# Kernel optimization log

Hardware: AMD Instinct MI355X
Metric: run time of the kernel (lower is better)

## Reference

```python
import jax, jax.numpy as jnp
import numpy as np

B, C, N, L, LAYERS = 32, 128, 307, 12, 4
LH = L + 1  # high-frequency channel time length after left-pad
BN_EPS = 1e-5


def _temporal_attention(seq, c1w, c2w, w, b, v, gamma, beta):
    # seq: [B, C, N, T]
    # conv1 (1x1 over channel dim) -> f1: [B, T, N]
    f1 = jnp.einsum('bcnt,c->btn', seq, c1w)
    # conv2 (1x1 over node dim)    -> f2: [B, T, C]
    f2 = jnp.einsum('bcnt,n->btc', seq, c2w)
    # scores = sigmoid(f1 @ w @ f2^T + b): [B, T, T]
    f1w = jnp.einsum('btn,nc->btc', f1, w)
    scores = jax.nn.sigmoid(jnp.einsum('btc,bqc->btq', f1w, f2) + b)
    # learned mixing: v @ scores
    logits = jnp.einsum('tk,bkq->btq', v, scores)
    # BatchNorm1d over tem_size channels (channel = last axis q after the
    # permute(0,2,1) in the torch code); training-mode batch statistics
    mean = logits.mean(axis=(0, 1), keepdims=True)
    var = ((logits - mean) ** 2).mean(axis=(0, 1), keepdims=True)
    logits = (logits - mean) * jax.lax.rsqrt(var + BN_EPS) * gamma + beta
    coefs = jax.nn.softmax(logits, axis=-1)  # [B, T, Q]
    # x_1 = einsum('bcnl,blq->bcnq', seq, coefs^T)
    return jnp.einsum('bcnt,bqt->bcnq', seq, coefs)


def _make_params(key, c, n, t, layers):
    ks = jax.random.split(key, 4)
    return dict(
        c1=jax.random.normal(ks[0], (layers, c), jnp.float32) * 0.05,
        c2=jax.random.normal(ks[1], (layers, n), jnp.float32) * 0.05,
        w=jax.random.normal(ks[2], (layers, n, c), jnp.float32) * 0.05,
        b=jnp.zeros((layers, t, t), jnp.float32),
        v=jax.random.normal(ks[3], (layers, t, t), jnp.float32) * 0.2,
        g=jnp.ones((layers, t), jnp.float32),
        beta=jnp.zeros((layers, t), jnp.float32),
    )


def setup_inputs():
    key = jax.random.key(0)
    k0, k1, k2, k3 = jax.random.split(key, 4)
    XL = jax.random.normal(k0, (B, C, N, L), jnp.float32)
    XH = jax.random.normal(k1, (B, C, N, L), jnp.float32)
    low = _make_params(k2, C, N, L, LAYERS)
    high = _make_params(k3, C, N, LH, LAYERS)
    return {
        'XL': XL, 'XH': XH,
        'low_c1': low['c1'], 'low_c2': low['c2'], 'low_w': low['w'],
        'low_b': low['b'], 'low_v': low['v'], 'low_g': low['g'], 'low_beta': low['beta'],
        'high_c1': high['c1'], 'high_c2': high['c2'], 'high_w': high['w'],
        'high_b': high['b'], 'high_v': high['v'], 'high_g': high['g'], 'high_beta': high['beta'],
        'alpha': jnp.array(-5.0, jnp.float32),
    }


def reference(XL, XH, low_c1, low_c2, low_w, low_b, low_v, low_g, low_beta,
              high_c1, high_c2, high_w, high_b, high_v, high_g, high_beta, alpha):
    res_xl, res_xh = XL, XH
    x = XL
    for i in range(LAYERS):
        x = _temporal_attention(x, low_c1[i], low_c2[i], low_w[i], low_b[i],
                                low_v[i], low_g[i], low_beta[i])
    xl = (res_xl[..., -1] + x[..., -1])[..., None]  # [B, C, N, 1]

    y = jnp.pad(XH, ((0, 0), (0, 0), (0, 0), (1, 0)))  # left-pad time -> [B,C,N,L+1]
    for i in range(LAYERS):
        y = _temporal_attention(y, high_c1[i], high_c2[i], high_w[i], high_b[i],
                                high_v[i], high_g[i], high_beta[i])
    xh = (res_xh[..., -1] + y[..., -1])[..., None]  # [B, C, N, 1]

    a = jax.nn.sigmoid(alpha)
    return a * xl + (1.0 - a) * xh
```

## Files before the change

kernel.cpp:

```cpp
#include <hip/hip_runtime.h>

#define Bn 32
#define Cc 128
#define Nn 307
#define Ll 12
#define LH 13
#define LAYERS 4
#define BN_EPS 1e-5f
#define SCW (Cc + 1)
#define G1SZ ((size_t)2 * LAYERS * Bn * LH * Nn)

#define NT1 16
__global__ __launch_bounds__(256, 4) void k_g1(const float* __restrict__ XL,
                                               const float* __restrict__ XH,
                                               const float* __restrict__ lc1,
                                               const float* __restrict__ hc1,
                                               float* __restrict__ G1) {
    __shared__ float s_c1[LAYERS * Cc];
    __shared__ float sred[12 * 260];
    int tile = blockIdx.x;
    int b = blockIdx.y;
    int ch = blockIdx.z;
    const float* X = ch ? XH : XL;
    const float* c1 = ch ? hc1 : lc1;
    int tid = threadIdx.x;
    for (int j = tid; j < LAYERS * Cc; j += 256) s_c1[j] = c1[j];
    __syncthreads();
    int nl = tid & 15;
    int l = (tid >> 4) & 3;
    int cs = tid >> 6;
    int n = tile * NT1 + nl;
    float4 a0 = {0.f, 0.f, 0.f, 0.f}, a1 = a0, a2 = a0;
    if (n < Nn) {
        const float* px = X + ((size_t)(b * Cc + cs * 32) * Nn + n) * Ll;
        const float* wp = s_c1 + l * Cc + cs * 32;
#pragma unroll 4
        for (int cc = 0; cc < 32; ++cc) {
            float4 v0 = *(const float4*)(px);
            float4 v1 = *(const float4*)(px + 4);
            float4 v2 = *(const float4*)(px + 8);
            float wv = wp[cc];
            a0.x += v0.x * wv; a0.y += v0.y * wv; a0.z += v0.z * wv; a0.w += v0.w * wv;
            a1.x += v1.x * wv; a1.y += v1.y * wv; a1.z += v1.z * wv; a1.w += v1.w * wv;
            a2.x += v2.x * wv; a2.y += v2.y * wv; a2.z += v2.z * wv; a2.w += v2.w * wv;
            px += (size_t)Nn * Ll;
        }
    }
    int g = tid & 63;
    float av[12] = {a0.x, a0.y, a0.z, a0.w, a1.x, a1.y,
                    a1.z, a1.w, a2.x, a2.y, a2.z, a2.w};
#pragma unroll
    for (int t = 0; t < 12; ++t) sred[t * 260 + cs * 64 + g] = av[t];
    __syncthreads();
#pragma unroll
    for (int r = 0; r < 3; ++r) {
        int o = r * 256 + tid;
        int og = o & 63, t = o >> 6;
        float v = sred[t * 260 + og] + sred[t * 260 + 64 + og] +
                  sred[t * 260 + 128 + og] + sred[t * 260 + 192 + og];
        int onl = og & 15, ol = og >> 4;
        int nn = tile * NT1 + onl;
        int t0 = ch ? (t + 1) : t;
        if (nn < Nn)
            G1[((size_t)(ch * LAYERS + ol) * Bn + b) * (LH * Nn) + (size_t)t0 * Nn + nn] = v;
    }
    if (tid < 64) {
        int onl = tid & 15, ol = tid >> 4;
        int nn = tile * NT1 + onl;
        int t0z = ch ? 0 : (LH - 1);
        if (nn < Nn)
            G1[((size_t)(ch * LAYERS + ol) * Bn + b) * (LH * Nn) + (size_t)t0z * Nn + nn] = 0.f;
    }
}

__global__ __launch_bounds__(256, 4) void k_g2(const float* __restrict__ XL,
                                               const float* __restrict__ XH,
                                               const float* __restrict__ lc2,
                                               const float* __restrict__ hc2,
                                               float* __restrict__ G2) {
    __shared__ float s_c2[LAYERS * Nn];
    __shared__ float sred[12 * 260];
    int ctile = blockIdx.x;
    int b = blockIdx.y;
    int ch = blockIdx.z;
    const float* X = ch ? XH : XL;
    const float* c2 = ch ? hc2 : lc2;
    int tid = threadIdx.x;
    for (int j = tid; j < LAYERS * Nn; j += 256) s_c2[j] = c2[j];
    __syncthreads();
    int c8 = tid & 7;
    int l = (tid >> 3) & 3;
    int ns = tid >> 5;
    int c = ctile * 8 + c8;
    float4 a0 = {0.f, 0.f, 0.f, 0.f}, a1 = a0, a2 = a0;
    const float* pb = X + (size_t)(b * Cc + c) * Nn * Ll;
    const float* wp = s_c2 + l * Nn;
#pragma unroll 4
    for (int n = ns; n < Nn; n += 8) {
        const float* px = pb + (size_t)n * Ll;
        float4 v0 = *(const float4*)(px);
        float4 v1 = *(const float4*)(px + 4);
        float4 v2 = *(const float4*)(px + 8);
        float wv = wp[n];
        a0.x += v0.x * wv; a0.y += v0.y * wv; a0.z += v0.z * wv; a0.w += v0.w * wv;
        a1.x += v1.x * wv; a1.y += v1.y * wv; a1.z += v1.z * wv; a1.w += v1.w * wv;
        a2.x += v2.x * wv; a2.y += v2.y * wv; a2.z += v2.z * wv; a2.w += v2.w * wv;
    }
    float av[12] = {a0.x, a0.y, a0.z, a0.w, a1.x, a1.y,
                    a1.z, a1.w, a2.x, a2.y, a2.z, a2.w};
#pragma unroll
    for (int t = 0; t < 12; ++t) sred[t * 260 + tid] = av[t];
    __syncthreads();
    size_t cb;
#pragma unroll
    for (int r = 0; r < 2; ++r) {
        int o = r * 256 + tid;
        if (o < 384) {
            int og = o & 31, t = o >> 5;
            float v = 0.f;
#pragma unroll
            for (int s = 0; s < 8; ++s) v += sred[t * 260 + s * 32 + og];
            int oc8 = og & 7, ol = og >> 3;
            int t0 = ch ? (t + 1) : t;
            G2[((size_t)(ch * LAYERS + ol) * Bn + b) * (LH * Cc) + (size_t)t0 * Cc +
               ctile * 8 + oc8] = v;
        }
    }
    if (ch && tid < 32) {
        int oc8 = tid & 7, ol = tid >> 3;
        G2[((size_t)(ch * LAYERS + ol) * Bn + b) * (LH * Cc) + ctile * 8 + oc8] = 0.f;
    }
}

#define GWR 4
__global__ __launch_bounds__(256) void k_gw(const float* __restrict__ lw,
                                            const float* __restrict__ hw,
                                            const float* __restrict__ G1,
                                            float* __restrict__ GW) {
    __shared__ float sG1[GWR * Nn];
    __shared__ float sred[8][GWR][Cc];
    int tile = blockIdx.x;
    int chl = blockIdx.y;
    int ch = chl >> 2, l = chl & 3;
    const float* w = (ch ? hw : lw) + (size_t)l * Nn * Cc;
    const float* g1 = G1 + (size_t)chl * Bn * (LH * Nn) + (size_t)tile * GWR * Nn;
    int tid = threadIdx.x;
    for (int i = tid; i < GWR * Nn / 4; i += 256)
        ((float4*)sG1)[i] = ((const float4*)g1)[i];
    __syncthreads();
    int c4 = (tid & 31) * 4;
    int stripe = tid >> 5;
    float4 a0 = {0.f, 0.f, 0.f, 0.f}, a1 = a0, a2 = a0, a3 = a0;
#define GW_FMA(wv, nn)                                         \
    {                                                          \
        float g0 = sG1[0 * Nn + (nn)];                         \
        float g1v = sG1[1 * Nn + (nn)];                        \
        float g2v = sG1[2 * Nn + (nn)];                        \
        float g3v = sG1[3 * Nn + (nn)];                        \
        a0.x += wv.x * g0;  a0.y += wv.y * g0;                 \
        a0.z += wv.z * g0;  a0.w += wv.w * g0;                 \
        a1.x += wv.x * g1v; a1.y += wv.y * g1v;                \
        a1.z += wv.z * g1v; a1.w += wv.w * g1v;                \
        a2.x += wv.x * g2v; a2.y += wv.y * g2v;                \
        a2.z += wv.z * g2v; a2.w += wv.w * g2v;                \
        a3.x += wv.x * g3v; a3.y += wv.y * g3v;                \
        a3.z += wv.z * g3v; a3.w += wv.w * g3v;                \
    }
    int n = stripe;
    for (; n + 24 < Nn; n += 32) {
        float4 w0 = *(const float4*)(w + (size_t)n * Cc + c4);
        float4 w1 = *(const float4*)(w + (size_t)(n + 8) * Cc + c4);
        float4 w2 = *(const float4*)(w + (size_t)(n + 16) * Cc + c4);
        float4 w3 = *(const float4*)(w + (size_t)(n + 24) * Cc + c4);
        GW_FMA(w0, n);
        GW_FMA(w1, n + 8);
        GW_FMA(w2, n + 16);
        GW_FMA(w3, n + 24);
    }
    for (; n < Nn; n += 8) {
        float4 w0 = *(const float4*)(w + (size_t)n * Cc + c4);
        GW_FMA(w0, n);
    }
#undef GW_FMA
    *(float4*)&sred[stripe][0][c4] = a0;
    *(float4*)&sred[stripe][1][c4] = a1;
    *(float4*)&sred[stripe][2][c4] = a2;
    *(float4*)&sred[stripe][3][c4] = a3;
    __syncthreads();
    float* out = GW + (size_t)chl * Bn * (LH * Cc) + (size_t)tile * GWR * Cc;
    for (int o = tid; o < GWR * Cc; o += 256) {
        int r = o >> 7, cc = o & 127;
        float v = 0.f;
#pragma unroll
        for (int s = 0; s < 8; ++s) v += sred[s][r][cc];
        out[o] = v;
    }
}

__global__ __launch_bounds__(256) void k_m(const float* __restrict__ GW,
                                           const float* __restrict__ G2,
                                           float* __restrict__ M) {
    __shared__ float sGW[LH][SCW];
    __shared__ float sG2[LH][SCW];
    int blk = blockIdx.x;
    int ch = blk >> 7;
    int T = ch ? LH : Ll;
    const float* gw = GW + (size_t)blk * (LH * Cc);
    const float* g2 = G2 + (size_t)blk * (LH * Cc);
    int tid = threadIdx.x;
    for (int i = tid; i < LH * Cc; i += 256) {
        int t = i >> 7, c = i & 127;
        sGW[t][c] = gw[i];
        sG2[t][c] = g2[i];
    }
    __syncthreads();
    float* Mo = M + (size_t)blk * (LH * LH);
    for (int i = tid; i < T * T; i += 256) {
        int t0 = i / T, t1 = i % T;
        float a = 0.f;
#pragma unroll 8
        for (int cc = 0; cc < Cc; ++cc) a += sGW[t0][cc] * sG2[t1][cc];
        Mo[t0 * LH + t1] = a;
    }
}

template <int T>
__device__ __forceinline__ void first_impl(int ch, int b,
                                           const float* __restrict__ M,
                                           const float* __restrict__ bb,
                                           const float* __restrict__ v,
                                           float* __restrict__ Lg,
                                           float* __restrict__ Stats) {
    const int TT = T * T;
    __shared__ float sS[LH * LH];
    __shared__ float sA[LH * LH];
    int tid = threadIdx.x;
    const float* Ml = M + ((size_t)(ch * LAYERS + 0) * Bn + b) * (LH * LH);
    if (tid < TT) {
        int t = tid / T, q = tid % T;
        float a = bb[tid] + Ml[t * LH + q];
        sS[tid] = 1.f / (1.f + expf(-a));
    }
    __syncthreads();
    if (tid < TT) {
        int t = tid / T, q = tid % T;
        float a = 0.f;
#pragma unroll
        for (int k = 0; k < T; ++k) a += v[t * T + k] * sS[k * T + q];
        sA[tid] = a;
        Lg[(size_t)(ch * Bn + b) * (LH * LH) + tid] = a;
    }
    __syncthreads();
    if (tid < T) {
        float s = 0.f, ss = 0.f;
#pragma unroll
        for (int t = 0; t < T; ++t) {
            float x = sA[t * T + tid];
            s += x;
            ss += x * x;
        }
        float* St = Stats + (size_t)(0 * 2 + ch) * 2 * (LH * Bn);
        St[tid * Bn + b] = s;
        St[LH * Bn + tid * Bn + b] = ss;
    }
}

__global__ __launch_bounds__(192) void k_first(const float* __restrict__ M,
                                               const float* __restrict__ lb,
                                               const float* __restrict__ lv,
                                               const float* __restrict__ hb,
                                               const float* __restrict__ hv,
                                               float* __restrict__ Lg,
                                               float* __restrict__ Stats) {
    int ch = blockIdx.x >> 5, b = blockIdx.x & 31;
    if (ch == 0)
        first_impl<Ll>(0, b, M, lb, lv, Lg, Stats);
    else
        first_impl<LH>(1, b, M, hb, hv, Lg, Stats);
}

template <int T>
__device__ __forceinline__ void mid_impl(int ch, int b, int l,
                                         const float* __restrict__ M,
                                         const float* __restrict__ bb_all,
                                         const float* __restrict__ v_all,
                                         const float* __restrict__ g_all,
                                         const float* __restrict__ be_all,
                                         float* __restrict__ Lg,
                                         float* __restrict__ Stats,
                                         float* __restrict__ Pws) {
    const int TT = T * T;
    __shared__ float sP[LH * LH], sC[LH * LH], sA[LH * LH], sB[LH * LH], sM[LH * LH];
    __shared__ float sMean[LH], sScale[LH], sShift[LH];
    int tid = threadIdx.x;
    bool first = (l == 0);
    float* Lgb = Lg + (size_t)(ch * Bn + b) * (LH * LH);
    float* Pb = Pws + (size_t)(ch * Bn + b) * (LH * LH);
    if (tid < T) {
        const float* St = Stats + (size_t)(l * 2 + ch) * 2 * (LH * Bn);
        float s = 0.f, ss = 0.f;
        for (int b2 = 0; b2 < Bn; ++b2) {
            s += St[tid * Bn + b2];
            ss += St[LH * Bn + tid * Bn + b2];
        }
        float inv = 1.f / (float)(Bn * T);
        float m = s * inv;
        float var = ss * inv - m * m;
        sMean[tid] = m;
        sScale[tid] = rsqrtf(var + BN_EPS) * g_all[l * T + tid];
        sShift[tid] = be_all[l * T + tid];
    }
    if (tid < TT) {
        sA[tid] = Lgb[tid];
        if (!first) sP[tid] = Pb[tid];
    }
    __syncthreads();
    if (tid < T) {
        float vals[T];
        float mx = -1e30f;
#pragma unroll
        for (int q = 0; q < T; ++q) {
            float x = (sA[tid * T + q] - sMean[q]) * sScale[q] + sShift[q];
            vals[q] = x;
            mx = fmaxf(mx, x);
        }
        float sm = 0.f;
#pragma unroll
        for (int q = 0; q < T; ++q) {
            vals[q] = expf(vals[q] - mx);
            sm += vals[q];
        }
        float inv = 1.f / sm;
#pragma unroll
        for (int q = 0; q < T; ++q) sC[tid * T + q] = vals[q] * inv;
    }
    __syncthreads();
    if (tid < TT) {
        int t0 = tid / T, q = tid % T;
        float a;
        if (first) {
            a = sC[q * T + t0];
        } else {
            a = 0.f;
#pragma unroll
            for (int t = 0; t < T; ++t) a += sP[t0 * T + t] * sC[q * T + t];
        }
        sB[tid] = a;
        Pb[tid] = a;
    }
    const float* Mn = M + ((size_t)(ch * LAYERS + l + 1) * Bn + b) * (LH * LH);
    for (int i = tid; i < T * LH; i += 192) sM[i] = Mn[i];
    __syncthreads();
    if (tid < TT) {
        int t = tid / T, t1 = tid % T;
        float a = 0.f;
#pragma unroll
        for (int t0 = 0; t0 < T; ++t0) a += sB[t0 * T + t] * sM[t0 * LH + t1];
        sA[tid] = a;
    }
    __syncthreads();
    const float* bbn = bb_all + (size_t)(l + 1) * TT;
    if (tid < TT) {
        int t = tid / T, q = tid % T;
        float a = bbn[tid];
#pragma unroll
        for (int t1 = 0; t1 < T; ++t1) a += sA[t * T + t1] * sB[t1 * T + q];
        sP[tid] = 1.f / (1.f + expf(-a));
    }
    __syncthreads();
    const float* vn = v_all + (size_t)(l + 1) * TT;
    if (tid < TT) {
        int t = tid / T, q = tid % T;
        float a = 0.f;
#pragma unroll
        for (int k = 0; k < T; ++k) a += vn[t * T + k] * sP[k * T + q];
        sA[tid] = a;
        Lgb[tid] = a;
    }
    __syncthreads();
    if (tid < T) {
        float s = 0.f, ss = 0.f;
#pragma unroll
        for (int t = 0; t < T; ++t) {
            float x = sA[t * T + tid];
            s += x;
            ss += x * x;
        }
        float* St = Stats + (size_t)((l + 1) * 2 + ch) * 2 * (LH * Bn);
        St[tid * Bn + b] = s;
        St[LH * Bn + tid * Bn + b] = ss;
    }
}

__global__ __launch_bounds__(192) void k_mid(const float* __restrict__ M,
                                             const float* __restrict__ lb,
                                             const float* __restrict__ lv,
                                             const float* __restrict__ lgam,
                                             const float* __restrict__ lbet,
                                             const float* __restrict__ hb,
                                             const float* __restrict__ hv,
                                             const float* __restrict__ hgam,
                                             const float* __restrict__ hbet,
                                             float* __restrict__ Lg,
                                             float* __restrict__ Stats,
                                             float* __restrict__ Pws, int l) {
    int ch = blockIdx.x >> 5, b = blockIdx.x & 31;
    if (ch == 0)
        mid_impl<Ll>(0, b, l, M, lb, lv, lgam, lbet, Lg, Stats, Pws);
    else
        mid_impl<LH>(1, b, l, M, hb, hv, hgam, hbet, Lg, Stats, Pws);
}

template <int T>
__device__ __forceinline__ void last_impl(int ch, int b,
                                          const float* __restrict__ g_all,
                                          const float* __restrict__ be_all,
                                          const float* __restrict__ Lg,
                                          const float* __restrict__ Stats,
                                          const float* __restrict__ Pws,
                                          float* __restrict__ Pcol) {
    const int TT = T * T;
    const int l = LAYERS - 1;
    __shared__ float sP[LH * LH], sC[LH * LH], sA[LH * LH], sB[LH * LH];
    __shared__ float sMean[LH], sScale[LH], sShift[LH];
    int tid = threadIdx.x;
    const float* Lgb = Lg + (size_t)(ch * Bn + b) * (LH * LH);
    const float* Pb = Pws + (size_t)(ch * Bn + b) * (LH * LH);
    if (tid < T) {
        const float* St = Stats + (size_t)(l * 2 + ch) * 2 * (LH * Bn);
        float s = 0.f, ss = 0.f;
        for (int b2 = 0; b2 < Bn; ++b2) {
            s += St[tid * Bn + b2];
            ss += St[LH * Bn + tid * Bn + b2];
        }
        float inv = 1.f / (float)(Bn * T);
        float m = s * inv;
        float var = ss * inv - m * m;
        sMean[tid] = m;
        sScale[tid] = rsqrtf(var + BN_EPS) * g_all[l * T + tid];
        sShift[tid] = be_all[l * T + tid];
    }
    if (tid < TT) {
        sA[tid] = Lgb[tid];
        sP[tid] = Pb[tid];
    }
    __syncthreads();
    if (tid < T) {
        float vals[T];
        float mx = -1e30f;
#pragma unroll
        for (int q = 0; q < T; ++q) {
            float x = (sA[tid * T + q] - sMean[q]) * sScale[q] + sShift[q];
            vals[q] = x;
            mx = fmaxf(mx, x);
        }
        float sm = 0.f;
#pragma unroll
        for (int q = 0; q < T; ++q) {
            vals[q] = expf(vals[q] - mx);
            sm += vals[q];
        }
        float inv = 1.f / sm;
#pragma unroll
        for (int q = 0; q < T; ++q) sC[tid * T + q] = vals[q] * inv;
    }
    __syncthreads();
    if (tid < TT) {
        int t0 = tid / T, q = tid % T;
        float a = 0.f;
#pragma unroll
        for (int t = 0; t < T; ++t) a += sP[t0 * T + t] * sC[q * T + t];
        sB[tid] = a;
    }
    __syncthreads();
    if (tid < T) Pcol[(size_t)ch * Bn * LH + b * LH + tid] = sB[tid * T + (T - 1)];
}

__global__ __launch_bounds__(192) void k_last(const float* __restrict__ lgam,
                                              const float* __restrict__ lbet,
                                              const float* __restrict__ hgam,
                                              const float* __restrict__ hbet,
                                              const float* __restrict__ Lg,
                                              const float* __restrict__ Stats,
                                              const float* __restrict__ Pws,
                                              float* __restrict__ Pcol) {
    int ch = blockIdx.x >> 5, b = blockIdx.x & 31;
    if (ch == 0)
        last_impl<Ll>(0, b, lgam, lbet, Lg, Stats, Pws, Pcol);
    else
        last_impl<LH>(1, b, hgam, hbet, Lg, Stats, Pws, Pcol);
}

__global__ __launch_bounds__(256) void k_final(const float* __restrict__ XL,
                                               const float* __restrict__ XH,
                                               const float* __restrict__ Pcol,
                                               const float* __restrict__ alpha,
                                               float* __restrict__ out) {
    __shared__ float s_pl[Ll];
    __shared__ float s_ph[LH];
    int b = blockIdx.y;
    int tid = threadIdx.x;
    if (tid < Ll) s_pl[tid] = Pcol[b * LH + tid];
    if (tid < LH) s_ph[tid] = Pcol[Bn * LH + b * LH + tid];
    __syncthreads();
    int cn = blockIdx.x * blockDim.x + tid;
    if (cn >= Cc * Nn) return;
    size_t idx = (size_t)b * Cc * Nn + cn;
    const float* pl = XL + idx * Ll;
    const float* ph = XH + idx * Ll;
    float accL = 0.f, accH = 0.f;
#pragma unroll
    for (int t = 0; t < Ll; ++t) {
        accL += pl[t] * s_pl[t];
        accH += ph[t] * s_ph[t + 1];
    }
    float a = 1.f / (1.f + expf(-alpha[0]));
    float xl = pl[Ll - 1] + accL;
    float xh = ph[Ll - 1] + accH;
    out[idx] = a * xl + (1.f - a) * xh;
}

extern "C" void kernel_launch(void* const* d_in, const int* in_sizes, int n_in,
                              void* d_out, int out_size, void* d_ws, size_t ws_size,
                              hipStream_t stream) {
    const float* XL = (const float*)d_in[0];
    const float* XH = (const float*)d_in[1];
    const float* lc1 = (const float*)d_in[2];
    const float* lc2 = (const float*)d_in[3];
    const float* lw = (const float*)d_in[4];
    const float* lb = (const float*)d_in[5];
    const float* lv = (const float*)d_in[6];
    const float* lg = (const float*)d_in[7];
    const float* lbeta = (const float*)d_in[8];
    const float* hc1 = (const float*)d_in[9];
    const float* hc2 = (const float*)d_in[10];
    const float* hw = (const float*)d_in[11];
    const float* hb = (const float*)d_in[12];
    const float* hv = (const float*)d_in[13];
    const float* hg = (const float*)d_in[14];
    const float* hbeta = (const float*)d_in[15];
    const float* alpha = (const float*)d_in[16];
    float* out = (float*)d_out;

    float* ws = (float*)d_ws;
    float* G1 = ws;
    float* G2 = G1 + G1SZ;
    float* M = G2 + (size_t)2 * LAYERS * Bn * LH * Cc;
    float* Pcol = M + (size_t)2 * LAYERS * Bn * LH * LH;
    float* Stats = Pcol + (size_t)2 * Bn * LH;
    float* Lg = Stats + (size_t)4 * LAYERS * LH * Bn;
    float* Pws = Lg + (size_t)2 * Bn * LH * LH;
    float* GW = Pws + (size_t)2 * Bn * LH * LH;

    k_g1<<<dim3(20, 32, 2), 256, 0, stream>>>(XL, XH, lc1, hc1, G1);
    k_g2<<<dim3(16, 32, 2), 256, 0, stream>>>(XL, XH, lc2, hc2, G2);
    k_gw<<<dim3(104, 8), 256, 0, stream>>>(lw, hw, G1, GW);
    k_m<<<256, 256, 0, stream>>>(GW, G2, M);
    k_first<<<64, 192, 0, stream>>>(M, lb, lv, hb, hv, Lg, Stats);
    k_mid<<<64, 192, 0, stream>>>(M, lb, lv, lg, lbeta, hb, hv, hg, hbeta, Lg, Stats, Pws, 0);
    k_mid<<<64, 192, 0, stream>>>(M, lb, lv, lg, lbeta, hb, hv, hg, hbeta, Lg, Stats, Pws, 1);
    k_mid<<<64, 192, 0, stream>>>(M, lb, lv, lg, lbeta, hb, hv, hg, hbeta, Lg, Stats, Pws, 2);
    k_last<<<64, 192, 0, stream>>>(lg, lbeta, hg, hbeta, Lg, Stats, Pws, Pcol);
    k_final<<<dim3((Cc * Nn + 255) / 256, Bn), 256, 0, stream>>>(XL, XH, Pcol, alpha, out);
}
```

Baseline: 272.9 us.

## Coalesce X reads in g1, g2 and final kernels via flat float4 indexing

```diff
diff --git a/kernel.cpp b/kernel.cpp
--- a/kernel.cpp
+++ b/kernel.cpp
@@ -9,126 +9,142 @@
 #define BN_EPS 1e-5f
 #define SCW (Cc + 1)
 #define G1SZ ((size_t)2 * LAYERS * Bn * LH * Nn)
-
-#define NT1 16
-__global__ __launch_bounds__(256, 4) void k_g1(const float* __restrict__ XL,
-                                               const float* __restrict__ XH,
-                                               const float* __restrict__ lc1,
-                                               const float* __restrict__ hc1,
-                                               float* __restrict__ G1) {
-    __shared__ float s_c1[LAYERS * Cc];
-    __shared__ float sred[12 * 260];
-    int tile = blockIdx.x;
-    int b = blockIdx.y;
-    int ch = blockIdx.z;
+#define NF4 921
+
+__global__ __launch_bounds__(256) void k_g1(const float* __restrict__ XL,
+                                            const float* __restrict__ XH,
+                                            const float* __restrict__ lc1,
+                                            const float* __restrict__ hc1,
+                                            float* __restrict__ G1) {
+    __shared__ float s_c1t[Cc * 4];
+    int bx = blockIdx.x;
+    int ft = bx & 3, cs = bx >> 2;
+    int b = blockIdx.y, ch = blockIdx.z;
     const float* X = ch ? XH : XL;
     const float* c1 = ch ? hc1 : lc1;
     int tid = threadIdx.x;
-    for (int j = tid; j < LAYERS * Cc; j += 256) s_c1[j] = c1[j];
-    __syncthreads();
-    int nl = tid & 15;
-    int l = (tid >> 4) & 3;
-    int cs = tid >> 6;
-    int n = tile * NT1 + nl;
-    float4 a0 = {0.f, 0.f, 0.f, 0.f}, a1 = a0, a2 = a0;
-    if (n < Nn) {
-        const float* px = X + ((size_t)(b * Cc + cs * 32) * Nn + n) * Ll;
-        const float* wp = s_c1 + l * Cc + cs * 32;
-#pragma unroll 4
-        for (int cc = 0; cc < 32; ++cc) {
-            float4 v0 = *(const float4*)(px);
-            float4 v1 = *(const float4*)(px + 4);
-            float4 v2 = *(const float4*)(px + 8);
-            float wv = wp[cc];
-            a0.x += v0.x * wv; a0.y += v0.y * wv; a0.z += v0.z * wv; a0.w += v0.w * wv;
-            a1.x += v1.x * wv; a1.y += v1.y * wv; a1.z += v1.z * wv; a1.w += v1.w * wv;
-            a2.x += v2.x * wv; a2.y += v2.y * wv; a2.z += v2.z * wv; a2.w += v2.w * wv;
-            px += (size_t)Nn * Ll;
-        }
-    }
-    int g = tid & 63;
-    float av[12] = {a0.x, a0.y, a0.z, a0.w, a1.x, a1.y,
-                    a1.z, a1.w, a2.x, a2.y, a2.z, a2.w};
-#pragma unroll
-    for (int t = 0; t < 12; ++t) sred[t * 260 + cs * 64 + g] = av[t];
-    __syncthreads();
-#pragma unroll
-    for (int r = 0; r < 3; ++r) {
-        int o = r * 256 + tid;
-        int og = o & 63, t = o >> 6;
-        float v = sred[t * 260 + og] + sred[t * 260 + 64 + og] +
-                  sred[t * 260 + 128 + og] + sred[t * 260 + 192 + og];
-        int onl = og & 15, ol = og >> 4;
-        int nn = tile * NT1 + onl;
-        int t0 = ch ? (t + 1) : t;
-        if (nn < Nn)
-            G1[((size_t)(ch * LAYERS + ol) * Bn + b) * (LH * Nn) + (size_t)t0 * Nn + nn] = v;
-    }
-    if (tid < 64) {
-        int onl = tid & 15, ol = tid >> 4;
-        int nn = tile * NT1 + onl;
-        int t0z = ch ? 0 : (LH - 1);
-        if (nn < Nn)
-            G1[((size_t)(ch * LAYERS + ol) * Bn + b) * (LH * Nn) + (size_t)t0z * Nn + nn] = 0.f;
-    }
-}
-
-__global__ __launch_bounds__(256, 4) void k_g2(const float* __restrict__ XL,
-                                               const float* __restrict__ XH,
-                                               const float* __restrict__ lc2,
-                                               const float* __restrict__ hc2,
-                                               float* __restrict__ G2) {
-    __shared__ float s_c2[LAYERS * Nn];
-    __shared__ float sred[12 * 260];
-    int ctile = blockIdx.x;
-    int b = blockIdx.y;
-    int ch = blockIdx.z;
+    for (int j = tid; j < Cc * 4; j += 256) s_c1t[j] = c1[(j & 3) * Cc + (j >> 2)];
+    __syncthreads();
+    int f = ft * 256 + tid;
+    bool act = f < NF4;
+    int cbase = cs * 64;
+    float4 a0 = {0.f, 0.f, 0.f, 0.f}, a1 = a0, a2 = a0, a3 = a0;
+#define FMA16(xq, cidx)                                                        \
+    {                                                                          \
+        float4 wq = *(const float4*)&s_c1t[(cbase + (cidx)) * 4];              \
+        a0.x += xq.x * wq.x; a0.y += xq.y * wq.x; a0.z += xq.z * wq.x; a0.w += xq.w * wq.x; \
+        a1.x += xq.x * wq.y; a1.y += xq.y * wq.y; a1.z += xq.z * wq.y; a1.w += xq.w * wq.y; \
+        a2.x += xq.x * wq.z; a2.y += xq.y * wq.z; a2.z += xq.z * wq.z; a2.w += xq.w * wq.z; \
+        a3.x += xq.x * wq.w; a3.y += xq.y * wq.w; a3.z += xq.z * wq.w; a3.w += xq.w * wq.w; \
+    }
+    if (act) {
+        const float4* px = (const float4*)X + (size_t)(b * Cc + cbase) * NF4 + f;
+        float4 q0 = px[0], q1 = px[NF4], q2 = px[2 * NF4], q3 = px[3 * NF4];
+        px += 4 * NF4;
+        for (int c = 0; c < 56; c += 4) {
+            FMA16(q0, c);     q0 = px[0];
+            FMA16(q1, c + 1); q1 = px[NF4];
+            FMA16(q2, c + 2); q2 = px[2 * NF4];
+            FMA16(q3, c + 3); q3 = px[3 * NF4];
+            px += 4 * NF4;
+        }
+        FMA16(q0, 56); float4 r0 = px[0];
+        FMA16(q1, 57); float4 r1 = px[NF4];
+        FMA16(q2, 58); float4 r2 = px[2 * NF4];
+        FMA16(q3, 59); float4 r3 = px[3 * NF4];
+        FMA16(r0, 60); FMA16(r1, 61); FMA16(r2, 62); FMA16(r3, 63);
+    }
+#undef FMA16
+    float* Gout = G1 + (size_t)cs * G1SZ;
+    if (act) {
+        int tg = f % 3, nn = f / 3;
+        int t0b = 4 * tg + ch;
+        size_t base = ((size_t)(ch * LAYERS) * Bn + b) * (LH * Nn) + (size_t)t0b * Nn + nn;
+        const size_t ls = (size_t)Bn * LH * Nn;
+        Gout[base + 0 * ls + 0 * Nn] = a0.x; Gout[base + 0 * ls + 1 * Nn] = a0.y;
+        Gout[base + 0 * ls + 2 * Nn] = a0.z; Gout[base + 0 * ls + 3 * Nn] = a0.w;
+        Gout[base + 1 * ls + 0 * Nn] = a1.x; Gout[base + 1 * ls + 1 * Nn] = a1.y;
+        Gout[base + 1 * ls + 2 * Nn] = a1.z; Gout[base + 1 * ls + 3 * Nn] = a1.w;
+        Gout[base + 2 * ls + 0 * Nn] = a2.x; Gout[base + 2 * ls + 1 * Nn] = a2.y;
+        Gout[base + 2 * ls + 2 * Nn] = a2.z; Gout[base + 2 * ls + 3 * Nn] = a2.w;
+        Gout[base + 3 * ls + 0 * Nn] = a3.x; Gout[base + 3 * ls + 1 * Nn] = a3.y;
+        Gout[base + 3 * ls + 2 * Nn] = a3.z; Gout[base + 3 * ls + 3 * Nn] = a3.w;
+    }
+    int n0 = (ft * 256) / 3;
+    int n1 = (ft * 256 + 255) / 3; if (n1 > 306) n1 = 306;
+    int cnt = n1 - n0 + 1;
+    int t0z = ch ? 0 : (LH - 1);
+    for (int o = tid; o < 4 * cnt; o += 256) {
+        int l = o / cnt, nn = n0 + o % cnt;
+        Gout[((size_t)(ch * LAYERS + l) * Bn + b) * (LH * Nn) + (size_t)t0z * Nn + nn] = 0.f;
+    }
+}
+
+__global__ __launch_bounds__(192) void k_g2(const float* __restrict__ XL,
+                                            const float* __restrict__ XH,
+                                            const float* __restrict__ lc2,
+                                            const float* __restrict__ hc2,
+                                            float* __restrict__ G2) {
+    __shared__ float s_c2t[Nn * 4];
+    __shared__ float sred2[4 * 12 * 64];
+    int c = blockIdx.x, b = blockIdx.y, ch = blockIdx.z;
     const float* X = ch ? XH : XL;
     const float* c2 = ch ? hc2 : lc2;
     int tid = threadIdx.x;
-    for (int j = tid; j < LAYERS * Nn; j += 256) s_c2[j] = c2[j];
-    __syncthreads();
-    int c8 = tid & 7;
-    int l = (tid >> 3) & 3;
-    int ns = tid >> 5;
-    int c = ctile * 8 + c8;
-    float4 a0 = {0.f, 0.f, 0.f, 0.f}, a1 = a0, a2 = a0;
-    const float* pb = X + (size_t)(b * Cc + c) * Nn * Ll;
-    const float* wp = s_c2 + l * Nn;
-#pragma unroll 4
-    for (int n = ns; n < Nn; n += 8) {
-        const float* px = pb + (size_t)n * Ll;
-        float4 v0 = *(const float4*)(px);
-        float4 v1 = *(const float4*)(px + 4);
-        float4 v2 = *(const float4*)(px + 8);
-        float wv = wp[n];
-        a0.x += v0.x * wv; a0.y += v0.y * wv; a0.z += v0.z * wv; a0.w += v0.w * wv;
-        a1.x += v1.x * wv; a1.y += v1.y * wv; a1.z += v1.z * wv; a1.w += v1.w * wv;
-        a2.x += v2.x * wv; a2.y += v2.y * wv; a2.z += v2.z * wv; a2.w += v2.w * wv;
-    }
-    float av[12] = {a0.x, a0.y, a0.z, a0.w, a1.x, a1.y,
-                    a1.z, a1.w, a2.x, a2.y, a2.z, a2.w};
-#pragma unroll
-    for (int t = 0; t < 12; ++t) sred[t * 260 + tid] = av[t];
-    __syncthreads();
-    size_t cb;
-#pragma unroll
-    for (int r = 0; r < 2; ++r) {
-        int o = r * 256 + tid;
-        if (o < 384) {
-            int og = o & 31, t = o >> 5;
-            float v = 0.f;
-#pragma unroll
-            for (int s = 0; s < 8; ++s) v += sred[t * 260 + s * 32 + og];
-            int oc8 = og & 7, ol = og >> 3;
-            int t0 = ch ? (t + 1) : t;
-            G2[((size_t)(ch * LAYERS + ol) * Bn + b) * (LH * Cc) + (size_t)t0 * Cc +
-               ctile * 8 + oc8] = v;
-        }
-    }
-    if (ch && tid < 32) {
-        int oc8 = tid & 7, ol = tid >> 3;
-        G2[((size_t)(ch * LAYERS + ol) * Bn + b) * (LH * Cc) + ctile * 8 + oc8] = 0.f;
+    for (int j = tid; j < Nn * 4; j += 192) s_c2t[j] = c2[(j & 3) * Nn + (j >> 2)];
+    __syncthreads();
+    const float4* pb = (const float4*)X + (size_t)(b * Cc + c) * NF4;
+    float4 x0 = pb[tid];
+    float4 x1 = pb[tid + 192];
+    float4 x2 = pb[tid + 384];
+    float4 x3 = pb[tid + 576];
+    float4 x4 = {0.f, 0.f, 0.f, 0.f};
+    if (tid + 768 < NF4) x4 = pb[tid + 768];
+    float4 a0 = {0.f, 0.f, 0.f, 0.f}, a1 = a0, a2 = a0, a3 = a0;
+#define PROC(xq, ff)                                                           \
+    {                                                                          \
+        int n = (ff) / 3; if (n > 306) n = 306;                                \
+        float4 wq = *(const float4*)&s_c2t[n * 4];                             \
+        a0.x += xq.x * wq.x; a0.y += xq.y * wq.x; a0.z += xq.z * wq.x; a0.w += xq.w * wq.x; \
+        a1.x += xq.x * wq.y; a1.y += xq.y * wq.y; a1.z += xq.z * wq.y; a1.w += xq.w * wq.y; \
+        a2.x += xq.x * wq.z; a2.y += xq.y * wq.z; a2.z += xq.z * wq.z; a2.w += xq.w * wq.z; \
+        a3.x += xq.x * wq.w; a3.y += xq.y * wq.w; a3.z += xq.z * wq.w; a3.w += xq.w * wq.w; \
+    }
+    PROC(x0, tid);
+    PROC(x1, tid + 192);
+    PROC(x2, tid + 384);
+    PROC(x3, tid + 576);
+    PROC(x4, tid + 768);
+#undef PROC
+    int tg = tid % 3, m = tid / 3;
+    sred2[(0 * 12 + 4 * tg + 0) * 64 + m] = a0.x;
+    sred2[(0 * 12 + 4 * tg + 1) * 64 + m] = a0.y;
+    sred2[(0 * 12 + 4 * tg + 2) * 64 + m] = a0.z;
+    sred2[(0 * 12 + 4 * tg + 3) * 64 + m] = a0.w;
+    sred2[(1 * 12 + 4 * tg + 0) * 64 + m] = a1.x;
+    sred2[(1 * 12 + 4 * tg + 1) * 64 + m] = a1.y;
+    sred2[(1 * 12 + 4 * tg + 2) * 64 + m] = a1.z;
+    sred2[(1 * 12 + 4 * tg + 3) * 64 + m] = a1.w;
+    sred2[(2 * 12 + 4 * tg + 0) * 64 + m] = a2.x;
+    sred2[(2 * 12 + 4 * tg + 1) * 64 + m] = a2.y;
+    sred2[(2 * 12 + 4 * tg + 2) * 64 + m] = a2.z;
+    sred2[(2 * 12 + 4 * tg + 3) * 64 + m] = a2.w;
+    sred2[(3 * 12 + 4 * tg + 0) * 64 + m] = a3.x;
+    sred2[(3 * 12 + 4 * tg + 1) * 64 + m] = a3.y;
+    sred2[(3 * 12 + 4 * tg + 2) * 64 + m] = a3.z;
+    sred2[(3 * 12 + 4 * tg + 3) * 64 + m] = a3.w;
+    __syncthreads();
+    if (tid < 48) {
+        int l = tid / 12, t = tid % 12;
+        const float* r = &sred2[(l * 12 + t) * 64];
+        float v = 0.f;
+#pragma unroll 16
+        for (int k = 0; k < 64; ++k) v += r[k];
+        int t0 = t + ch;
+        G2[((size_t)(ch * LAYERS + l) * Bn + b) * (LH * Cc) + (size_t)t0 * Cc + c] = v;
+    } else if (ch && tid < 52) {
+        int l = tid - 48;
+        G2[((size_t)(ch * LAYERS + l) * Bn + b) * (LH * Cc) + c] = 0.f;
     }
 }
 
@@ -143,10 +159,15 @@
     int chl = blockIdx.y;
     int ch = chl >> 2, l = chl & 3;
     const float* w = (ch ? hw : lw) + (size_t)l * Nn * Cc;
-    const float* g1 = G1 + (size_t)chl * Bn * (LH * Nn) + (size_t)tile * GWR * Nn;
-    int tid = threadIdx.x;
-    for (int i = tid; i < GWR * Nn / 4; i += 256)
-        ((float4*)sG1)[i] = ((const float4*)g1)[i];
+    size_t g1off = (size_t)chl * Bn * (LH * Nn) + (size_t)tile * GWR * Nn;
+    const float4* g1a = (const float4*)(G1 + g1off);
+    const float4* g1b = (const float4*)(G1 + G1SZ + g1off);
+    int tid = threadIdx.x;
+    for (int i = tid; i < GWR * Nn / 4; i += 256) {
+        float4 pa = g1a[i], pb = g1b[i];
+        float4 s = {pa.x + pb.x, pa.y + pb.y, pa.z + pb.z, pa.w + pb.w};
+        ((float4*)sG1)[i] = s;
+    }
     __syncthreads();
     int c4 = (tid & 31) * 4;
     int stripe = tid >> 5;
@@ -491,33 +512,38 @@
         last_impl<LH>(1, b, hgam, hbet, Lg, Stats, Pws, Pcol);
 }
 
-__global__ __launch_bounds__(256) void k_final(const float* __restrict__ XL,
+__global__ __launch_bounds__(192) void k_final(const float* __restrict__ XL,
                                                const float* __restrict__ XH,
                                                const float* __restrict__ Pcol,
                                                const float* __restrict__ alpha,
                                                float* __restrict__ out) {
     __shared__ float s_pl[Ll];
     __shared__ float s_ph[LH];
+    __shared__ float sfin[192];
     int b = blockIdx.y;
     int tid = threadIdx.x;
     if (tid < Ll) s_pl[tid] = Pcol[b * LH + tid];
-    if (tid < LH) s_ph[tid] = Pcol[Bn * LH + b * LH + tid];
-    __syncthreads();
-    int cn = blockIdx.x * blockDim.x + tid;
-    if (cn >= Cc * Nn) return;
-    size_t idx = (size_t)b * Cc * Nn + cn;
-    const float* pl = XL + idx * Ll;
-    const float* ph = XH + idx * Ll;
-    float accL = 0.f, accH = 0.f;
-#pragma unroll
-    for (int t = 0; t < Ll; ++t) {
-        accL += pl[t] * s_pl[t];
-        accH += ph[t] * s_ph[t + 1];
-    }
+    if (tid >= 64 && tid < 64 + LH) s_ph[tid - 64] = Pcol[Bn * LH + b * LH + (tid - 64)];
+    __syncthreads();
+    int F = blockIdx.x * 192 + tid;
+    int tg = F % 3;
+    const float4* pl4 = (const float4*)XL + (size_t)b * (Cc * Nn * 3) + F;
+    const float4* ph4 = (const float4*)XH + (size_t)b * (Cc * Nn * 3) + F;
+    float4 xl = *pl4;
+    float4 xh = *ph4;
     float a = 1.f / (1.f + expf(-alpha[0]));
-    float xl = pl[Ll - 1] + accL;
-    float xh = ph[Ll - 1] + accH;
-    out[idx] = a * xl + (1.f - a) * xh;
+    const float* wl = &s_pl[4 * tg];
+    const float* wh = &s_ph[4 * tg + 1];
+    float pL = xl.x * wl[0] + xl.y * wl[1] + xl.z * wl[2] + xl.w * wl[3];
+    float pH = xh.x * wh[0] + xh.y * wh[1] + xh.z * wh[2] + xh.w * wh[3];
+    float p = a * pL + (1.f - a) * pH;
+    if (tg == 2) p += a * xl.w + (1.f - a) * xh.w;
+    sfin[tid] = p;
+    __syncthreads();
+    if (tid < 64) {
+        float v = sfin[3 * tid] + sfin[3 * tid + 1] + sfin[3 * tid + 2];
+        out[(size_t)b * (Cc * Nn) + blockIdx.x * 64 + tid] = v;
+    }
 }
 
 extern "C" void kernel_launch(void* const* d_in, const int* in_sizes, int n_in,
@@ -544,7 +570,7 @@
 
     float* ws = (float*)d_ws;
     float* G1 = ws;
-    float* G2 = G1 + G1SZ;
+    float* G2 = G1 + 2 * G1SZ;
     float* M = G2 + (size_t)2 * LAYERS * Bn * LH * Cc;
     float* Pcol = M + (size_t)2 * LAYERS * Bn * LH * LH;
     float* Stats = Pcol + (size_t)2 * Bn * LH;
@@ -552,8 +578,8 @@
     float* Pws = Lg + (size_t)2 * Bn * LH * LH;
     float* GW = Pws + (size_t)2 * Bn * LH * LH;
 
-    k_g1<<<dim3(20, 32, 2), 256, 0, stream>>>(XL, XH, lc1, hc1, G1);
-    k_g2<<<dim3(16, 32, 2), 256, 0, stream>>>(XL, XH, lc2, hc2, G2);
+    k_g1<<<dim3(8, 32, 2), 256, 0, stream>>>(XL, XH, lc1, hc1, G1);
+    k_g2<<<dim3(128, 32, 2), 192, 0, stream>>>(XL, XH, lc2, hc2, G2);
     k_gw<<<dim3(104, 8), 256, 0, stream>>>(lw, hw, G1, GW);
     k_m<<<256, 256, 0, stream>>>(GW, G2, M);
     k_first<<<64, 192, 0, stream>>>(M, lb, lv, hb, hv, Lg, Stats);
@@ -561,5 +587,5 @@
     k_mid<<<64, 192, 0, stream>>>(M, lb, lv, lg, lbeta, hb, hv, hg, hbeta, Lg, Stats, Pws, 1);
     k_mid<<<64, 192, 0, stream>>>(M, lb, lv, lg, lbeta, hb, hv, hg, hbeta, Lg, Stats, Pws, 2);
     k_last<<<64, 192, 0, stream>>>(lg, lbeta, hg, hbeta, Lg, Stats, Pws, Pcol);
-    k_final<<<dim3((Cc * Nn + 255) / 256, Bn), 256, 0, stream>>>(XL, XH, Pcol, alpha, out);
-}
+    k_final<<<dim3(614, 32), 192, 0, stream>>>(XL, XH, Pcol, alpha, out);
+}
```

Result: faster. 256.5 us (-6.0%).
